# Optimization experiments

Measured on AMD Instinct MI355X. Metric: run time of the kernel, lower is better.

## Reference

```python
import jax, jax.numpy as jnp
import numpy as np

OUTPUT_SIZE = 16384          # number of map units (must be a perfect square)
SIDE = 128.0                 # sqrt(OUTPUT_SIZE)
SIGMA = 2.0                  # neighbourhood std-dev (non-trainable weight in original)
B, D = 2048, 256


def setup_inputs() -> dict:
    key = jax.random.key(0)
    k1, k2 = jax.random.split(key)
    x = jax.random.normal(k1, (B, D), dtype=jnp.float32)
    kernel = jax.random.normal(k2, (D, OUTPUT_SIZE), dtype=jnp.float32) * 0.1
    return {"x": x, "kernel": kernel}


def _grid_coords():
    # 2D coordinates of each flattened map unit: unit k -> (k // side, k % side)
    idx = jnp.arange(OUTPUT_SIZE, dtype=jnp.float32)
    return jnp.floor(idx / SIDE), jnp.mod(idx, SIDE)  # each (size,)


def reference(x, kernel):
    # Squared Euclidean distance of every sample to every prototype: (B, size).
    # Same math as tf.norm(x[:, :, None] - kernel[None])**2, expressed as a GEMM.
    norms2 = (jnp.sum(x * x, axis=1, keepdims=True)
              - 2.0 * (x @ kernel)
              + jnp.sum(kernel * kernel, axis=0, keepdims=True))
    norms2 = jnp.maximum(norms2, 0.0)

    # Winner-take-all unit per sample, mapped to 2D grid coordinates.
    wta = jnp.argmin(norms2, axis=1).astype(jnp.float32)        # (B,)
    mean_r = jnp.floor(wta / SIDE)                               # (B,)
    mean_c = jnp.mod(wta, SIDE)                                  # (B,)

    # Gaussian neighbourhood over the 2D grid, flattened: (B, size).
    gr, gc = _grid_coords()
    dr = gr[None, :] - mean_r[:, None]
    dc = gc[None, :] - mean_c[:, None]
    radials = jnp.exp(-0.5 / (SIGMA * SIGMA) * (dr * dr + dc * dc))

    return radials * norms2
```

## Files before the change

### kernel.cpp

```cpp
#include <hip/hip_runtime.h>
#include <hip/hip_fp16.h>

#define OUTN 16384
#define BATCH 2048
#define DIM   256

typedef _Float16 half8 __attribute__((ext_vector_type(8)));
typedef _Float16 half4 __attribute__((ext_vector_type(4)));
typedef float    floatx4 __attribute__((ext_vector_type(4)));
typedef unsigned long long u64;

__device__ __forceinline__ void gl2lds16(const void* g, void* l) {
    __builtin_amdgcn_global_load_lds(
        (const __attribute__((address_space(1))) void*)g,
        (__attribute__((address_space(3))) void*)l, 16, 0, 0);
}

__device__ __forceinline__ u64 packkey(float v, int col) {
    unsigned u = __float_as_uint(v);
    u = (u & 0x80000000u) ? ~u : (u | 0x80000000u);
    return ((u64)u << 32) | (unsigned)col;
}
__device__ __forceinline__ float unpackval(u64 p) {
    unsigned u = (unsigned)(p >> 32);
    u = (u & 0x80000000u) ? (u & 0x7fffffffu) : ~u;
    return __uint_as_float(u);
}

__global__ __launch_bounds__(256) void prep_all(
        const float* __restrict__ x, const float* __restrict__ kern,
        _Float16* __restrict__ xh, float* __restrict__ rown,
        _Float16* __restrict__ kT, float* __restrict__ colnp,
        float* __restrict__ kT32) {
    int blk = blockIdx.x, t = threadIdx.x;
    if (blk < 512) {
        __shared__ float tile[64][65];
        __shared__ float npart[4][64];
        int tx = t & 63, ty = t >> 6;
        int j0 = (blk >> 1) * 64;
        int dhalf = blk & 1, dbase = dhalf * 128;
        float nrm = 0.f;
        for (int pc = 0; pc < 2; pc++) {
            int dc = dbase + pc * 64;
            __syncthreads();
            for (int it = 0; it < 16; it++) {
                int d = dc + ty + it * 4;
                float v = kern[(size_t)d * OUTN + j0 + tx];
                tile[ty + it * 4][tx] = v;
                nrm = fmaf(v, v, nrm);
            }
            __syncthreads();
            for (int c = t; c < 512; c += 256) {
                int j = c >> 3, o8 = (c & 7) * 8;
                half8 h;
                for (int u = 0; u < 8; u++) h[u] = (_Float16)tile[o8 + u][j];
                *(half8*)&kT[(size_t)(j0 + j) * DIM + dc + o8] = h;
            }
            if (kT32) {
                for (int c = t; c < 1024; c += 256) {
                    int j = c >> 4, o4 = (c & 15) * 4;
                    float4 f = make_float4(tile[o4][j], tile[o4 + 1][j],
                                           tile[o4 + 2][j], tile[o4 + 3][j]);
                    *(float4*)&kT32[(size_t)(j0 + j) * DIM + dc + o4] = f;
                }
            }
        }
        npart[ty][tx] = nrm;
        __syncthreads();
        if (t < 64)
            colnp[(size_t)dhalf * OUTN + j0 + t] =
                npart[0][t] + npart[1][t] + npart[2][t] + npart[3][t];
    } else {
        int b = blk - 512;
        float v = x[b * DIM + t];
        xh[b * DIM + t] = (_Float16)v;
        float s = v * v;
        for (int off = 32; off; off >>= 1) s += __shfl_down(s, off, 64);
        __shared__ float wsum[4];
        if ((t & 63) == 0) wsum[t >> 6] = s;
        __syncthreads();
        if (t == 0) rown[b] = wsum[0] + wsum[1] + wsum[2] + wsum[3];
    }
}

template <bool NF16>
__global__ __launch_bounds__(256) void gemm_norms(
        const _Float16* __restrict__ xh, const _Float16* __restrict__ kT,
        const float* __restrict__ rown, const float* __restrict__ colnp,
        void* __restrict__ n2out, u64* __restrict__ blockcand) {
    __shared__ __align__(16) char smem[32768];
    _Float16* As = (_Float16*)smem;
    _Float16* Bs = (_Float16*)(smem + 16384);
    u64* cand = (u64*)smem;
    int tid  = threadIdx.x;
    int col0 = blockIdx.x * 128;
    int row0 = blockIdx.y * 128;
    int wid = tid >> 6, lane = tid & 63;
    int wr = wid >> 1, wc = wid & 1;
    int l15 = lane & 15, l4 = lane >> 4;
    int xh7 = l15 & 7;

    floatx4 acc[4][4];
    for (int i = 0; i < 4; i++)
        for (int j = 0; j < 4; j++)
            acc[i][j] = (floatx4){0.f, 0.f, 0.f, 0.f};

    for (int kt = 0; kt < 4; kt++) {
        int k0 = kt * 64;
        for (int it = 0; it < 4; it++) {
            int chunk = it * 256 + tid;
            int r = chunk >> 3, gg = chunk & 7;
            int ksw = (gg ^ (r & 7)) * 8;
            gl2lds16(&xh[(size_t)(row0 + r) * DIM + k0 + ksw], &As[chunk * 8]);
            gl2lds16(&kT[(size_t)(col0 + r) * DIM + k0 + ksw], &Bs[chunk * 8]);
        }
        __syncthreads();
        for (int s = 0; s < 2; s++) {
            int g = s * 4 + l4;
            int sw = (g ^ xh7) * 8;
            half8 af[4], bf[4];
            for (int i = 0; i < 4; i++)
                af[i] = *(half8*)&As[(wr * 64 + i * 16 + l15) * 64 + sw];
            for (int j = 0; j < 4; j++)
                bf[j] = *(half8*)&Bs[(wc * 64 + j * 16 + l15) * 64 + sw];
            for (int i = 0; i < 4; i++)
                for (int j = 0; j < 4; j++)
                    acc[i][j] = __builtin_amdgcn_mfma_f32_16x16x32_f16(
                        af[i], bf[j], acc[i][j], 0, 0, 0);
        }
        __syncthreads();
    }

    float cn[4]; int oc[4];
    int cid = wc * 16 + l15;
    for (int j = 0; j < 4; j++) {
        oc[j] = col0 + wc * 64 + j * 16 + l15;
        cn[j] = colnp[oc[j]] + colnp[OUTN + oc[j]];
    }
    for (int i = 0; i < 4; i++) {
        for (int r = 0; r < 4; r++) {
            int row_l = wr * 64 + i * 16 + l4 * 4 + r;
            int orow  = row0 + row_l;
            float rn = rown[orow];
            u64 best = ~0ull;
            for (int j = 0; j < 4; j++) {
                float val = rn + cn[j] - 2.0f * acc[i][j][r];
                size_t oi = (size_t)orow * OUTN + oc[j];
                if (NF16) ((_Float16*)n2out)[oi] = (_Float16)val;
                else      ((float*)n2out)[oi]    = val;
                u64 p = packkey(val, oc[j]);
                if (p < best) best = p;
            }
            cand[row_l * 32 + (cid ^ (row_l & 31))] = best;
        }
    }
    __syncthreads();
    if (tid < 128) {
        u64 m1 = ~0ull, m2 = ~0ull;
        for (int s = 0; s < 32; s++) {
            u64 v = cand[tid * 32 + (s ^ (tid & 31))];
            if (v < m1) { m2 = m1; m1 = v; }
            else if (v < m2) { m2 = v; }
        }
        size_t base = (size_t)(row0 + tid) * 256 + blockIdx.x * 2;
        blockcand[base]     = m1;
        blockcand[base + 1] = m2;
    }
}

template <bool NF16, bool KT32P>
__global__ __launch_bounds__(256) void refine_finalize(
        const u64* __restrict__ blockcand, const float* __restrict__ x,
        const float* __restrict__ kern, const float* __restrict__ colnp,
        const float* __restrict__ kT32, const void* __restrict__ n2in,
        float* __restrict__ out) {
    int b = blockIdx.x, t = threadIdx.x;
    __shared__ float xrow[DIM];
    __shared__ u64 red[256];
    xrow[t] = x[b * DIM + t];
    u64 e = blockcand[(size_t)b * 256 + t];
    red[t] = e;
    __syncthreads();
    for (int off = 128; off; off >>= 1) {
        if (t < off) { u64 o = red[t + off]; if (o < red[t]) red[t] = o; }
        __syncthreads();
    }
    float minv = unpackval(red[0]);
    __syncthreads();

    float ve = unpackval(e);
    u64 p = ~0ull;
    if (ve <= minv + 0.125f) {
        int j = (int)(e & 0xffffffffu);
        float dot = 0.f;
        if (KT32P) {
            const float4* kc = (const float4*)&kT32[(size_t)j * DIM];
            for (int d4 = 0; d4 < DIM / 4; d4++) {
                float4 kv = kc[d4];
                dot = fmaf(xrow[d4 * 4 + 0], kv.x, dot);
                dot = fmaf(xrow[d4 * 4 + 1], kv.y, dot);
                dot = fmaf(xrow[d4 * 4 + 2], kv.z, dot);
                dot = fmaf(xrow[d4 * 4 + 3], kv.w, dot);
            }
        } else {
            for (int d = 0; d < DIM; d++)
                dot = fmaf(xrow[d], kern[(size_t)d * OUTN + j], dot);
        }
        p = packkey((colnp[j] + colnp[OUTN + j]) - 2.0f * dot, j);
    }
    red[t] = p;
    __syncthreads();
    for (int off = 128; off; off >>= 1) {
        if (t < off) { u64 o = red[t + off]; if (o < red[t]) red[t] = o; }
        __syncthreads();
    }
    int w = (int)(red[0] & 0xffffffffu);
    int wrr = w >> 7, wcc = w & 127;

    const _Float16* r16 = (const _Float16*)n2in + (size_t)b * OUTN;
    const float*    r32 = (const float*)n2in    + (size_t)b * OUTN;
    float* rowp = out + (size_t)b * OUTN;

    int c0 = (t & 31) * 4, rb = t >> 5;
    int dc0 = c0 - wcc;
    int q0 = dc0 * dc0, q1 = (dc0 + 1) * (dc0 + 1),
        q2 = (dc0 + 2) * (dc0 + 2), q3 = (dc0 + 3) * (dc0 + 3);
    int qmin = min(min(q0, q1), min(q2, q3));
    float ec0 = __expf(-0.125f * (float)q0), ec1 = __expf(-0.125f * (float)q1),
          ec2 = __expf(-0.125f * (float)q2), ec3 = __expf(-0.125f * (float)q3);

    for (int it = 0; it < 16; it++) {
        int idx4 = it * 256 + t;
        int r = it * 8 + rb;
        int dr = r - wrr, drsq = dr * dr;
        float4 res = make_float4(0.f, 0.f, 0.f, 0.f);
        if (drsq + qmin <= 720) {
            float va, vb, vc, vd;
            if (NF16) {
                half4 h = *(const half4*)&r16[idx4 * 4];
                va = (float)h[0]; vb = (float)h[1]; vc = (float)h[2]; vd = (float)h[3];
            } else {
                float4 f = ((const float4*)r32)[idx4];
                va = f.x; vb = f.y; vc = f.z; vd = f.w;
            }
            float er = __expf(-0.125f * (float)drsq);
            if (drsq + q0 <= 720) res.x = er * ec0 * fmaxf(va, 0.f);
            if (drsq + q1 <= 720) res.y = er * ec1 * fmaxf(vb, 0.f);
            if (drsq + q2 <= 720) res.z = er * ec2 * fmaxf(vc, 0.f);
            if (drsq + q3 <= 720) res.w = er * ec3 * fmaxf(vd, 0.f);
        }
        ((float4*)rowp)[idx4] = res;
    }
}

extern "C" void kernel_launch(void* const* d_in, const int* in_sizes, int n_in,
                              void* d_out, int out_size, void* d_ws, size_t ws_size,
                              hipStream_t stream) {
    const float* x    = (const float*)d_in[0];
    const float* kern = (const float*)d_in[1];
    float* out = (float*)d_out;
    char* ws = (char*)d_ws;

    _Float16* xh   = (_Float16*)(ws);
    _Float16* kT   = (_Float16*)(ws + (1u << 20));
    float*   colnp = (float*)(ws + (9u << 20));
    float*   rown  = (float*)(ws + (9u << 20) + (128u << 10));
    u64* blockcand = (u64*)(ws + (10u << 20));
    void*    n2h   = (void*)(ws + (14u << 20));
    bool f16path  = ws_size >= ((size_t)78 << 20);
    bool kt32path = ws_size >= ((size_t)94 << 20);
    float* kT32 = kt32path ? (float*)(ws + (78u << 20)) : nullptr;

    prep_all<<<2560, 256, 0, stream>>>(x, kern, xh, rown, kT, colnp, kT32);
    if (f16path) {
        gemm_norms<true><<<dim3(OUTN / 128, BATCH / 128), 256, 0, stream>>>(
            xh, kT, rown, colnp, n2h, blockcand);
        if (kt32path)
            refine_finalize<true, true><<<BATCH, 256, 0, stream>>>(
                blockcand, x, kern, colnp, kT32, n2h, out);
        else
            refine_finalize<true, false><<<BATCH, 256, 0, stream>>>(
                blockcand, x, kern, colnp, nullptr, n2h, out);
    } else {
        gemm_norms<false><<<dim3(OUTN / 128, BATCH / 128), 256, 0, stream>>>(
            xh, kT, rown, colnp, (void*)out, blockcand);
        refine_finalize<false, false><<<BATCH, 256, 0, stream>>>(
            blockcand, x, kern, colnp, nullptr, (const void*)out, out);
    }
}
```

Before: 200.2 us.

## Remap GEMM blocks per XCD, use nontemporal stores, wave-shuffle reductions

Remaps GEMM block IDs so each of the 8 XCDs owns a contiguous group of 16 column tiles, which improves L2 reuse of kernel tiles across row blocks. Switches the large norms2, output and kT32 writes to nontemporal stores to reduce cache pollution. Replaces the shared-memory tree argmin in refine_finalize with wave-level shuffle reductions that need fewer barriers, and splits the refine dot product across four accumulators. The remap assumes the grid is exactly 128x16 blocks and that blocks are dispatched round-robin across XCDs.

```diff
diff --git a/kernel.cpp b/kernel.cpp
--- a/kernel.cpp
+++ b/kernel.cpp
@@ -59,9 +59,10 @@
             if (kT32) {
                 for (int c = t; c < 1024; c += 256) {
                     int j = c >> 4, o4 = (c & 15) * 4;
-                    float4 f = make_float4(tile[o4][j], tile[o4 + 1][j],
-                                           tile[o4 + 2][j], tile[o4 + 3][j]);
-                    *(float4*)&kT32[(size_t)(j0 + j) * DIM + dc + o4] = f;
+                    floatx4 f = (floatx4){tile[o4][j], tile[o4 + 1][j],
+                                          tile[o4 + 2][j], tile[o4 + 3][j]};
+                    __builtin_nontemporal_store(f,
+                        (floatx4*)&kT32[(size_t)(j0 + j) * DIM + dc + o4]);
                 }
             }
         }
@@ -93,8 +94,12 @@
     _Float16* Bs = (_Float16*)(smem + 16384);
     u64* cand = (u64*)smem;
     int tid  = threadIdx.x;
-    int col0 = blockIdx.x * 128;
-    int row0 = blockIdx.y * 128;
+    int bid  = blockIdx.y * gridDim.x + blockIdx.x;
+    int xcd  = bid & 7, kk = bid >> 3;
+    int colblk = xcd * 16 + (kk & 15);
+    int rowblk = kk >> 4;
+    int col0 = colblk * 128;
+    int row0 = rowblk * 128;
     int wid = tid >> 6, lane = tid & 63;
     int wr = wid >> 1, wc = wid & 1;
     int l15 = lane & 15, l4 = lane >> 4;
@@ -146,8 +151,9 @@
             for (int j = 0; j < 4; j++) {
                 float val = rn + cn[j] - 2.0f * acc[i][j][r];
                 size_t oi = (size_t)orow * OUTN + oc[j];
-                if (NF16) ((_Float16*)n2out)[oi] = (_Float16)val;
-                else      ((float*)n2out)[oi]    = val;
+                if (NF16) __builtin_nontemporal_store((_Float16)val,
+                              (_Float16*)n2out + oi);
+                else      __builtin_nontemporal_store(val, (float*)n2out + oi);
                 u64 p = packkey(val, oc[j]);
                 if (p < best) best = p;
             }
@@ -162,7 +168,7 @@
             if (v < m1) { m2 = m1; m1 = v; }
             else if (v < m2) { m2 = v; }
         }
-        size_t base = (size_t)(row0 + tid) * 256 + blockIdx.x * 2;
+        size_t base = (size_t)(row0 + tid) * 256 + colblk * 2;
         blockcand[base]     = m1;
         blockcand[base + 1] = m2;
     }
@@ -176,45 +182,55 @@
         float* __restrict__ out) {
     int b = blockIdx.x, t = threadIdx.x;
     __shared__ float xrow[DIM];
-    __shared__ u64 red[256];
+    __shared__ u64 wred[4];
     xrow[t] = x[b * DIM + t];
     u64 e = blockcand[(size_t)b * 256 + t];
-    red[t] = e;
+
+    u64 m = e;
+    for (int off = 32; off; off >>= 1) {
+        u64 o = __shfl_xor(m, off, 64);
+        if (o < m) m = o;
+    }
+    if ((t & 63) == 0) wred[t >> 6] = m;
     __syncthreads();
-    for (int off = 128; off; off >>= 1) {
-        if (t < off) { u64 o = red[t + off]; if (o < red[t]) red[t] = o; }
-        __syncthreads();
-    }
-    float minv = unpackval(red[0]);
-    __syncthreads();
+    u64 g0 = wred[0] < wred[1] ? wred[0] : wred[1];
+    u64 g1 = wred[2] < wred[3] ? wred[2] : wred[3];
+    float minv = unpackval(g0 < g1 ? g0 : g1);
 
     float ve = unpackval(e);
     u64 p = ~0ull;
     if (ve <= minv + 0.125f) {
         int j = (int)(e & 0xffffffffu);
-        float dot = 0.f;
         if (KT32P) {
-            const float4* kc = (const float4*)&kT32[(size_t)j * DIM];
+            float d0 = 0.f, d1 = 0.f, d2 = 0.f, d3 = 0.f;
+            const floatx4* kc = (const floatx4*)&kT32[(size_t)j * DIM];
             for (int d4 = 0; d4 < DIM / 4; d4++) {
-                float4 kv = kc[d4];
-                dot = fmaf(xrow[d4 * 4 + 0], kv.x, dot);
-                dot = fmaf(xrow[d4 * 4 + 1], kv.y, dot);
-                dot = fmaf(xrow[d4 * 4 + 2], kv.z, dot);
-                dot = fmaf(xrow[d4 * 4 + 3], kv.w, dot);
-            }
+                floatx4 kv = kc[d4];
+                d0 = fmaf(xrow[d4 * 4 + 0], kv[0], d0);
+                d1 = fmaf(xrow[d4 * 4 + 1], kv[1], d1);
+                d2 = fmaf(xrow[d4 * 4 + 2], kv[2], d2);
+                d3 = fmaf(xrow[d4 * 4 + 3], kv[3], d3);
+            }
+            float dot = (d0 + d1) + (d2 + d3);
+            p = packkey((colnp[j] + colnp[OUTN + j]) - 2.0f * dot, j);
         } else {
+            float dot = 0.f;
             for (int d = 0; d < DIM; d++)
                 dot = fmaf(xrow[d], kern[(size_t)d * OUTN + j], dot);
-        }
-        p = packkey((colnp[j] + colnp[OUTN + j]) - 2.0f * dot, j);
-    }
-    red[t] = p;
+            p = packkey((colnp[j] + colnp[OUTN + j]) - 2.0f * dot, j);
+        }
+    }
     __syncthreads();
-    for (int off = 128; off; off >>= 1) {
-        if (t < off) { u64 o = red[t + off]; if (o < red[t]) red[t] = o; }
-        __syncthreads();
-    }
-    int w = (int)(red[0] & 0xffffffffu);
+    u64 m2 = p;
+    for (int off = 32; off; off >>= 1) {
+        u64 o = __shfl_xor(m2, off, 64);
+        if (o < m2) m2 = o;
+    }
+    if ((t & 63) == 0) wred[t >> 6] = m2;
+    __syncthreads();
+    u64 h0 = wred[0] < wred[1] ? wred[0] : wred[1];
+    u64 h1 = wred[2] < wred[3] ? wred[2] : wred[3];
+    int w = (int)((h0 < h1 ? h0 : h1) & 0xffffffffu);
     int wrr = w >> 7, wcc = w & 127;
 
     const _Float16* r16 = (const _Float16*)n2in + (size_t)b * OUTN;
@@ -233,23 +249,23 @@
         int idx4 = it * 256 + t;
         int r = it * 8 + rb;
         int dr = r - wrr, drsq = dr * dr;
-        float4 res = make_float4(0.f, 0.f, 0.f, 0.f);
+        floatx4 res = (floatx4){0.f, 0.f, 0.f, 0.f};
         if (drsq + qmin <= 720) {
             float va, vb, vc, vd;
             if (NF16) {
                 half4 h = *(const half4*)&r16[idx4 * 4];
                 va = (float)h[0]; vb = (float)h[1]; vc = (float)h[2]; vd = (float)h[3];
             } else {
-                float4 f = ((const float4*)r32)[idx4];
-                va = f.x; vb = f.y; vc = f.z; vd = f.w;
+                floatx4 f = ((const floatx4*)r32)[idx4];
+                va = f[0]; vb = f[1]; vc = f[2]; vd = f[3];
             }
             float er = __expf(-0.125f * (float)drsq);
-            if (drsq + q0 <= 720) res.x = er * ec0 * fmaxf(va, 0.f);
-            if (drsq + q1 <= 720) res.y = er * ec1 * fmaxf(vb, 0.f);
-            if (drsq + q2 <= 720) res.z = er * ec2 * fmaxf(vc, 0.f);
-            if (drsq + q3 <= 720) res.w = er * ec3 * fmaxf(vd, 0.f);
-        }
-        ((float4*)rowp)[idx4] = res;
+            if (drsq + q0 <= 720) res[0] = er * ec0 * fmaxf(va, 0.f);
+            if (drsq + q1 <= 720) res[1] = er * ec1 * fmaxf(vb, 0.f);
+            if (drsq + q2 <= 720) res[2] = er * ec2 * fmaxf(vc, 0.f);
+            if (drsq + q3 <= 720) res[3] = er * ec3 * fmaxf(vd, 0.f);
+        }
+        __builtin_nontemporal_store(res, (floatx4*)rowp + idx4);
     }
 }
 
```

Result: slower. 228.0 us (+13.9%).
